# Kernel optimization log

Measured on AMD Instinct MI355X. Metric: run time of the kernel, lower is better.

Reference implementation:

```python
import jax, jax.numpy as jnp
import numpy as np

N_NONZERO = 32      # n_nonzero_coefs
TAU = 0.01
LAMBDA_INIT = -5.0  # reg_coeff = softplus(lambda)


def setup_inputs() -> dict:
    key = jax.random.key(0)
    k1, k2 = jax.random.split(key)
    X = jax.random.normal(k1, (64, 1024, 1024), dtype=jnp.float32)
    y = jax.random.normal(k2, (64, 1024, 1), dtype=jnp.float32)
    return {"X": X, "y": y}


def _omp_fit_forward(X, y):
    # Faithful translation of fit() (omp with hard straight-through top-1)
    # followed by forward() reconstruction D @ coef.
    reg = jax.nn.softplus(jnp.asarray(LAMBDA_INIT, jnp.float32)).astype(X.dtype)
    B, L, A = X.shape
    ones = jnp.ones((B, L, 1), X.dtype)
    Dfull = jnp.concatenate([X, ones], axis=-1)   # [B, L, A+1] (bias column)
    D = Dfull[0]                                   # shared dictionary [L, A+1]
    n_atoms = A + 1
    y2 = y[:, :, 0]                                # [B, L]
    y_det = jax.lax.stop_gradient(y2)
    residuals = y_det
    # Cache selected_D columns incrementally: each column j is dict @ ret_j,
    # identical math to the original's full recompute every iteration.
    selD = jnp.zeros((B, L, N_NONZERO), X.dtype)
    idx_all = []
    nzW = None
    for i in range(N_NONZERO):
        proj = residuals @ D                                      # [B, A+1]
        soft = jax.nn.softmax(jnp.abs(proj) / TAU, axis=-1)
        idx = jnp.argmax(jnp.abs(proj), axis=-1)                  # detached indices
        onehot = jax.nn.one_hot(jnp.argmax(soft, axis=-1), n_atoms, dtype=X.dtype)
        ret = onehot - jax.lax.stop_gradient(soft) + soft         # straight-through
        new_col = ret @ D.T                                       # [B, L]
        selD = selD.at[:, :, i].set(new_col)
        Di = selD[:, :, :i + 1]                                   # [B, L, i+1]
        DTy = jnp.einsum('blk,bl->bk', Di, y2)[..., None]         # [B, i+1, 1]
        DTD = jnp.einsum('blk,blj->bkj', Di, Di) + reg * jnp.eye(i + 1, dtype=X.dtype)
        nzW = jnp.linalg.solve(DTD, DTy)                          # [B, i+1, 1]
        residuals = y_det - jnp.einsum('blk,bk->bl', Di, nzW[..., 0])
        idx_all.append(idx)
    indices = jnp.stack(idx_all, axis=1)                          # [B, K] int
    W = jnp.zeros((B, n_atoms), X.dtype).at[jnp.arange(B)[:, None], indices].set(nzW[..., 0])
    # forward(): bmm(dict_with_bias, coef)
    recon = jnp.einsum('bla,ba->bl', Dfull, W)[..., None]         # [B, L, 1]
    return recon


def reference(X, y):
    return _omp_fit_forward(X, y)
```

## Files before the change

### kernel.cpp

```cpp
#include <hip/hip_runtime.h>
#include <math.h>

#define NATOMS   1025
#define GSTRIDE  1040
#define GELEMS   (1025*GSTRIDE)
#define NNZ      32
#define NBATCH   64
#define REGL     0.0067153485f

#define DPPF(x, ctrl) __int_as_float(__builtin_amdgcn_update_dpp(0, __float_as_int(x), (ctrl), 0xF, 0xF, false))

__device__ __forceinline__ float wave_max64(float x) {
    x = fmaxf(x, DPPF(x, 0x111));
    x = fmaxf(x, DPPF(x, 0x112));
    x = fmaxf(x, DPPF(x, 0x114));
    x = fmaxf(x, DPPF(x, 0x118));
    x = fmaxf(x, DPPF(x, 0x142));
    x = fmaxf(x, DPPF(x, 0x143));
    return __int_as_float(__builtin_amdgcn_readlane(__float_as_int(x), 63));
}
__device__ __forceinline__ float wave_sum64(float x) {
    x += DPPF(x, 0x111);
    x += DPPF(x, 0x112);
    x += DPPF(x, 0x114);
    x += DPPF(x, 0x118);
    x += DPPF(x, 0x142);
    x += DPPF(x, 0x143);
    return __int_as_float(__builtin_amdgcn_readlane(__float_as_int(x), 63));
}
__device__ __forceinline__ float readlane_f(float x, int l) {
    return __int_as_float(__builtin_amdgcn_readlane(__float_as_int(x), l));
}

__global__ __launch_bounds__(256)
void gramprojy_kernel(const float* __restrict__ X0, const float* __restrict__ y,
                      float* __restrict__ Gout, float* __restrict__ PY,
                      int kLen, int nsplit) {
    __shared__ float lds[8192];
    const int tid = threadIdx.x;

    if ((int)blockIdx.z < nsplit) {
        const int bx = blockIdx.x, by = blockIdx.y, bz = blockIdx.z;
        if (by < bx) return;
        float* As = lds;
        float* Bs = lds + 4096;
        const int a0 = bx * 128, b0 = by * 128;
        float* __restrict__ Gp = Gout + (size_t)bz * GELEMS;
        const int tx = tid & 15;
        const int ty = tid >> 4;
        const int lr = tid >> 5;
        const int lc = (tid & 31) * 4;
        const bool aIn = (a0 + 128) <= 1024;
        const bool bIn = (b0 + 128) <= 1024;

        float acc[8][8];
#pragma unroll
        for (int m = 0; m < 8; ++m)
#pragma unroll
            for (int n = 0; n < 8; ++n) acc[m][n] = 0.0f;

        const int kBase = bz * kLen;
        for (int kc = 0; kc < kLen; kc += 32) {
#pragma unroll
            for (int rr = 0; rr < 4; ++rr) {
                const int r = lr + rr * 8;
                const int l = kBase + kc + r;
                if (aIn) {
                    *(float4*)&As[r * 128 + lc] = *(const float4*)&X0[(size_t)l * 1024 + a0 + lc];
                } else {
#pragma unroll
                    for (int k = 0; k < 4; ++k) {
                        const int col = a0 + lc + k;
                        As[r * 128 + lc + k] = (col < 1024) ? X0[(size_t)l * 1024 + col]
                                                            : (col == 1024 ? 1.0f : 0.0f);
                    }
                }
                if (bIn) {
                    *(float4*)&Bs[r * 128 + lc] = *(const float4*)&X0[(size_t)l * 1024 + b0 + lc];
                } else {
#pragma unroll
                    for (int k = 0; k < 4; ++k) {
                        const int col = b0 + lc + k;
                        Bs[r * 128 + lc + k] = (col < 1024) ? X0[(size_t)l * 1024 + col]
                                                            : (col == 1024 ? 1.0f : 0.0f);
                    }
                }
            }
            __syncthreads();
#pragma unroll 8
            for (int l = 0; l < 32; ++l) {
                float4 a01 = *(const float4*)&As[l * 128 + ty * 8];
                float4 a23 = *(const float4*)&As[l * 128 + ty * 8 + 4];
                float4 bA  = *(const float4*)&Bs[l * 128 + tx * 4];
                float4 bB  = *(const float4*)&Bs[l * 128 + 64 + tx * 4];
                float am[8] = {a01.x, a01.y, a01.z, a01.w, a23.x, a23.y, a23.z, a23.w};
                float bn[8] = {bA.x, bA.y, bA.z, bA.w, bB.x, bB.y, bB.z, bB.w};
#pragma unroll
                for (int m = 0; m < 8; ++m)
#pragma unroll
                    for (int n = 0; n < 8; ++n)
                        acc[m][n] += am[m] * bn[n];
            }
            __syncthreads();
        }

#pragma unroll
        for (int m = 0; m < 8; ++m) {
            const int a = a0 + ty * 8 + m;
            if (a >= NATOMS) continue;
            const int bAc = b0 + tx * 4;
            const int bBc = b0 + 64 + tx * 4;
            if (bAc < GSTRIDE) {
                *(float4*)&Gp[(size_t)a * GSTRIDE + bAc] =
                    make_float4(acc[m][0], acc[m][1], acc[m][2], acc[m][3]);
            }
            if (bBc < GSTRIDE) {
                *(float4*)&Gp[(size_t)a * GSTRIDE + bBc] =
                    make_float4(acc[m][4], acc[m][5], acc[m][6], acc[m][7]);
            }
        }
    } else {
        const int pw = blockIdx.y * 9 + blockIdx.x;
        if (pw >= 68) return;
        const int a0 = (pw % 17) * 64;
        const int b0 = (pw / 17) * 16;
        float* Ds = lds;
        float* Ys = lds + 2048;
        const int tx = tid & 15;
        const int ty = tid >> 4;
        const bool aIn = (a0 + 64) <= 1024;

        float acc[4] = {0.0f, 0.0f, 0.0f, 0.0f};

        for (int kc = 0; kc < 1024; kc += 32) {
            {
                const int r  = tid >> 4;
                const int c4 = (tid & 15) * 4;
#pragma unroll
                for (int rr = 0; rr < 2; ++rr) {
                    const int row = r + rr * 16;
                    const int l = kc + row;
                    if (aIn) {
                        *(float4*)&Ds[row * 64 + c4] = *(const float4*)&X0[(size_t)l * 1024 + a0 + c4];
                    } else {
#pragma unroll
                        for (int k = 0; k < 4; ++k) {
                            const int col = a0 + c4 + k;
                            Ds[row * 64 + c4 + k] = (col < 1024) ? X0[(size_t)l * 1024 + col]
                                                                 : (col == 1024 ? 1.0f : 0.0f);
                        }
                    }
                }
            }
            for (int e = tid; e < 512; e += 256) {
                const int l = e & 31, bb = e >> 5;
                Ys[l * 17 + bb] = y[(size_t)(b0 + bb) * 1024 + kc + l];
            }
            __syncthreads();
#pragma unroll 8
            for (int l = 0; l < 32; ++l) {
                const float yv = Ys[l * 17 + ty];
                float4 dv = *(const float4*)&Ds[l * 64 + tx * 4];
                acc[0] += yv * dv.x; acc[1] += yv * dv.y;
                acc[2] += yv * dv.z; acc[3] += yv * dv.w;
            }
            __syncthreads();
        }
        const int a = a0 + tx * 4;
        if (a < GSTRIDE) {
            *(float4*)&PY[(size_t)(b0 + ty) * GSTRIDE + a] =
                make_float4(acc[0], acc[1], acc[2], acc[3]);
        }
    }
}

__global__ __launch_bounds__(256)
void combine_kernel(const float* __restrict__ Gp, float* __restrict__ G,
                    float* __restrict__ diagG, int nsplit) {
    int tt = blockIdx.x, bx = 0;
    while (tt >= 9 - bx) { tt -= 9 - bx; ++bx; }
    const int by = bx + tt;
    const int yq = blockIdx.y;
    const int tid = threadIdx.x;
    for (int rep = 0; rep < 16; ++rep) {
        const int idx = yq * 4096 + rep * 256 + tid;
        const int r = idx >> 7, c = idx & 127;
        const int a = bx * 128 + r, b = by * 128 + c;
        if (a > 1024 || b > 1024) continue;
        float s = 0.0f;
        for (int z = 0; z < nsplit; ++z)
            s += Gp[(size_t)z * GELEMS + (size_t)a * GSTRIDE + b];
        G[(size_t)a * GSTRIDE + b] = s;
        G[(size_t)b * GSTRIDE + a] = s;
        if (a == b) diagG[a] = s;
    }
}

__global__ __launch_bounds__(512)
void omp_kernel(const float* __restrict__ G, const float* __restrict__ PY,
                const float* __restrict__ diagG,
                int* __restrict__ idxOut, float* __restrict__ wOut) {
    __shared__ float rowsLds[NNZ][GSTRIDE];
    __shared__ float pyLds[1040];
    __shared__ float diagLds[1040];
    __shared__ float redV[2][8];
    __shared__ int   redI[2][8];

    const int b = blockIdx.x, tid = threadIdx.x;
    const int lane = tid & 63, wid = tid >> 6;

    float ainv[32];
#pragma unroll
    for (int m = 0; m < 32; ++m) ainv[m] = 0.0f;
    float wvr = 0.0f, rhsr = 0.0f;
    int   myIdx = 0;
    float myW = 0.0f;

    {
        float4 z4 = make_float4(0.f, 0.f, 0.f, 0.f);
        float4* rz = (float4*)rowsLds;
        for (int u = tid; u < NNZ * GSTRIDE / 4; u += 512) rz[u] = z4;
        const float* pyg = PY + (size_t)b * GSTRIDE;
        for (int u = tid; u < 1040; u += 512) pyLds[u] = pyg[u];
        for (int u = tid; u < 1025; u += 512) diagLds[u] = diagG[u];
    }
    __syncthreads();

    float p0 = pyLds[tid], p1 = pyLds[tid + 512];
    float p2 = (tid == 511) ? pyLds[1024] : 0.0f;

    {
        float best = fabsf(p0); int bidx = tid;
        { float v = fabsf(p1); if (v > best) { best = v; bidx = tid + 512; } }
        if (tid == 511) { float v = fabsf(p2); if (v > best) { best = v; bidx = 1024; } }
        const float wmax = wave_max64(best);
        const unsigned long long mask = __ballot(best == wmax);
        const int fl = __ffsll((unsigned long long)mask) - 1;
        const int widx = __builtin_amdgcn_readlane(bidx, fl);
        if (lane == 0) { redV[0][wid] = wmax; redI[0][wid] = widx; }
    }
    __syncthreads();

    for (int i = 0; i < NNZ; ++i) {
        const int par = i & 1;

        float bv_ = redV[par][0]; int sel = redI[par][0];
#pragma unroll
        for (int q = 1; q < 8; ++q) {
            if (redV[par][q] > bv_ || (redV[par][q] == bv_ && redI[par][q] < sel)) {
                bv_ = redV[par][q]; sel = redI[par][q];
            }
        }
        const float pysel = pyLds[sel];

        float r0 = 0.f, r1 = 0.f, r2 = 0.f;
        const float* __restrict__ grow = G + (size_t)sel * GSTRIDE;
        if (i < NNZ - 1) {
            r0 = grow[tid];
            r1 = grow[tid + 512];
            if (tid == 511) r2 = grow[1024];
        }

        const float bvl = (lane < 32) ? rowsLds[lane][sel] : 0.0f;
        float u0 = 0.f, u1 = 0.f, u2 = 0.f, u3 = 0.f;
#pragma unroll
        for (int m = 0; m < 32; m += 4) {
            u0 = fmaf(ainv[m + 0], rowsLds[m + 0][sel], u0);
            u1 = fmaf(ainv[m + 1], rowsLds[m + 1][sel], u1);
            u2 = fmaf(ainv[m + 2], rowsLds[m + 2][sel], u2);
            u3 = fmaf(ainv[m + 3], rowsLds[m + 3][sel], u3);
        }
        const float uacc = (u0 + u1) + (u2 + u3);
        const float t = wave_sum64(bvl * uacc);
        const float s = wave_sum64(rhsr * uacc);
        const float dinv = 1.0f / (diagLds[sel] + REGL - t);
        const float beta = dinv * (pysel - s);
        const float uvb = (lane == i) ? -1.0f : uacc;
#pragma unroll
        for (int m = 0; m < 32; ++m)
            ainv[m] = fmaf(uvb * dinv, readlane_f(uvb, m), ainv[m]);
        wvr = (lane == i) ? beta : fmaf(-uacc, beta, wvr);
        rhsr = (lane == i) ? pysel : rhsr;
        if (tid == i) myIdx = sel;

        if (i == NNZ - 1) break;

        float z0 = -r0, z1 = -r1, z2 = -r2;
        for (int jb = 0; jb < NNZ; jb += 8) {
            if (jb >= i) break;
#pragma unroll
            for (int jj = 0; jj < 8; ++jj) {
                const int j = jb + jj;
                const float uj = readlane_f(uvb, j);
                z0 = fmaf(uj, rowsLds[j][tid],       z0);
                z1 = fmaf(uj, rowsLds[j][tid + 512], z1);
                if (tid == 511) z2 = fmaf(uj, rowsLds[j][1024], z2);
            }
        }
        p0 = fmaf(beta, z0, p0);
        p1 = fmaf(beta, z1, p1);
        if (tid == 511) p2 = fmaf(beta, z2, p2);

        rowsLds[i][tid]       = r0;
        rowsLds[i][tid + 512] = r1;
        if (tid == 511) rowsLds[i][1024] = r2;

        {
            float best = fabsf(p0); int bidx = tid;
            { float v = fabsf(p1); if (v > best) { best = v; bidx = tid + 512; } }
            if (tid == 511) { float v = fabsf(p2); if (v > best) { best = v; bidx = 1024; } }
            const float wmax = wave_max64(best);
            const unsigned long long mask = __ballot(best == wmax);
            const int fl = __ffsll((unsigned long long)mask) - 1;
            const int widx = __builtin_amdgcn_readlane(bidx, fl);
            if (lane == 0) { redV[par ^ 1][wid] = wmax; redI[par ^ 1][wid] = widx; }
        }
        __syncthreads();
    }

    if (tid < NNZ) {
        idxOut[b * NNZ + tid] = myIdx;
        wOut[b * NNZ + tid] = wvr;
    }
}

__global__ __launch_bounds__(256)
void recon_kernel(const float* __restrict__ X, const int* __restrict__ idxIn,
                  const float* __restrict__ wIn, float* __restrict__ out) {
    __shared__ float Wd[1025];
    __shared__ float wval[NNZ];
    __shared__ int   widx[NNZ];
    __shared__ float biasS;
    const int b = blockIdx.x >> 2, chunk = blockIdx.x & 3;
    const int tid = threadIdx.x;
    for (int u = tid; u < 1025; u += 256) Wd[u] = 0.0f;
    __syncthreads();
    if (tid == 0) {
#pragma unroll
        for (int i = 0; i < NNZ; ++i) Wd[idxIn[b * NNZ + i]] = wIn[b * NNZ + i];
        float bias = 0.0f;
#pragma unroll
        for (int i = 0; i < NNZ; ++i) {
            const int gi = idxIn[b * NNZ + i];
            const float v = Wd[gi];
            Wd[gi] = 0.0f;
            const bool isOnes = (gi == 1024);
            if (isOnes) bias += v;
            widx[i] = isOnes ? 0 : gi;
            wval[i] = isOnes ? 0.0f : v;
        }
        biasS = bias;
    }
    __syncthreads();
    const int l = chunk * 256 + tid;
    const float* __restrict__ xr = X + (size_t)b * 1024 * 1024 + (size_t)l * 1024;
    float a0 = biasS, a1 = 0.f, a2 = 0.f, a3 = 0.f;
#pragma unroll
    for (int i = 0; i < NNZ; i += 4) {
        a0 = fmaf(xr[widx[i + 0]], wval[i + 0], a0);
        a1 = fmaf(xr[widx[i + 1]], wval[i + 1], a1);
        a2 = fmaf(xr[widx[i + 2]], wval[i + 2], a2);
        a3 = fmaf(xr[widx[i + 3]], wval[i + 3], a3);
    }
    out[(size_t)b * 1024 + l] = (a0 + a1) + (a2 + a3);
}

extern "C" void kernel_launch(void* const* d_in, const int* in_sizes, int n_in,
                              void* d_out, int out_size, void* d_ws, size_t ws_size,
                              hipStream_t stream) {
    const float* X = (const float*)d_in[0];
    const float* y = (const float*)d_in[1];
    float* out = (float*)d_out;
    float* ws = (float*)d_ws;

    const size_t need4 = ((size_t)GELEMS * 5 + 64 * GSTRIDE + NBATCH * NNZ * 2 + 2048) * sizeof(float);
    const int nsplit = (ws_size >= need4) ? 4 : 1;
    const int kLen = 1024 / nsplit;

    float* Gp = ws;
    float* G  = ws + (size_t)GELEMS * nsplit;
    float* PY = G + (size_t)GELEMS;
    float* wOut = PY + (size_t)64 * GSTRIDE;
    int* idxOut = (int*)(wOut + NBATCH * NNZ);
    float* diagG = (float*)(idxOut + NBATCH * NNZ);

    gramprojy_kernel<<<dim3(9, 9, nsplit + 1), 256, 0, stream>>>(X, y, Gp, PY, kLen, nsplit);
    combine_kernel<<<dim3(45, 4), 256, 0, stream>>>(Gp, G, diagG, nsplit);
    omp_kernel<<<NBATCH, 512, 0, stream>>>(G, PY, diagG, idxOut, wOut);
    recon_kernel<<<NBATCH * 4, 256, 0, stream>>>(X, idxOut, wOut, out);
}
```

Baseline: 221.2 us.

## Drop combine kernel; sum split-K Gram partials on demand in OMP kernel

The separate combine kernel that reduced split-K Gram partials and symmetrized them is removed. The Gram kernel now writes the mirrored transpose tile directly for off-diagonal blocks, and the OMP kernel reads and sums the NS partial rows (and the diagonal) only for the rows it selects. The split count can also rise to 8 when workspace allows, which adds Gram parallelism. The cost is extra partial reads per selected row in the serial OMP loop and more partial buffer traffic.

```diff
diff --git a/kernel.cpp b/kernel.cpp
--- a/kernel.cpp
+++ b/kernel.cpp
@@ -119,6 +119,18 @@
                     make_float4(acc[m][4], acc[m][5], acc[m][6], acc[m][7]);
             }
         }
+        if (bx != by) {
+#pragma unroll
+            for (int n = 0; n < 8; ++n) {
+                const int colg = b0 + ((n < 4) ? (tx * 4 + n) : (64 + tx * 4 + (n - 4)));
+                if (colg >= NATOMS) continue;
+                const int a = a0 + ty * 8;
+                *(float4*)&Gp[(size_t)colg * GSTRIDE + a] =
+                    make_float4(acc[0][n], acc[1][n], acc[2][n], acc[3][n]);
+                *(float4*)&Gp[(size_t)colg * GSTRIDE + a + 4] =
+                    make_float4(acc[4][n], acc[5][n], acc[6][n], acc[7][n]);
+            }
+        }
     } else {
         const int pw = blockIdx.y * 9 + blockIdx.x;
         if (pw >= 68) return;
@@ -174,31 +186,9 @@
     }
 }
 
-__global__ __launch_bounds__(256)
-void combine_kernel(const float* __restrict__ Gp, float* __restrict__ G,
-                    float* __restrict__ diagG, int nsplit) {
-    int tt = blockIdx.x, bx = 0;
-    while (tt >= 9 - bx) { tt -= 9 - bx; ++bx; }
-    const int by = bx + tt;
-    const int yq = blockIdx.y;
-    const int tid = threadIdx.x;
-    for (int rep = 0; rep < 16; ++rep) {
-        const int idx = yq * 4096 + rep * 256 + tid;
-        const int r = idx >> 7, c = idx & 127;
-        const int a = bx * 128 + r, b = by * 128 + c;
-        if (a > 1024 || b > 1024) continue;
-        float s = 0.0f;
-        for (int z = 0; z < nsplit; ++z)
-            s += Gp[(size_t)z * GELEMS + (size_t)a * GSTRIDE + b];
-        G[(size_t)a * GSTRIDE + b] = s;
-        G[(size_t)b * GSTRIDE + a] = s;
-        if (a == b) diagG[a] = s;
-    }
-}
-
+template <int NS>
 __global__ __launch_bounds__(512)
-void omp_kernel(const float* __restrict__ G, const float* __restrict__ PY,
-                const float* __restrict__ diagG,
+void omp_kernel(const float* __restrict__ Gp, const float* __restrict__ PY,
                 int* __restrict__ idxOut, float* __restrict__ wOut) {
     __shared__ float rowsLds[NNZ][GSTRIDE];
     __shared__ float pyLds[1040];
@@ -214,7 +204,6 @@
     for (int m = 0; m < 32; ++m) ainv[m] = 0.0f;
     float wvr = 0.0f, rhsr = 0.0f;
     int   myIdx = 0;
-    float myW = 0.0f;
 
     {
         float4 z4 = make_float4(0.f, 0.f, 0.f, 0.f);
@@ -222,7 +211,17 @@
         for (int u = tid; u < NNZ * GSTRIDE / 4; u += 512) rz[u] = z4;
         const float* pyg = PY + (size_t)b * GSTRIDE;
         for (int u = tid; u < 1040; u += 512) pyLds[u] = pyg[u];
-        for (int u = tid; u < 1025; u += 512) diagLds[u] = diagG[u];
+        float d0 = 0.f, d1 = 0.f, d2 = 0.f;
+#pragma unroll
+        for (int z = 0; z < NS; ++z) {
+            const float* gz = Gp + (size_t)z * GELEMS;
+            d0 += gz[(size_t)tid * (GSTRIDE + 1)];
+            d1 += gz[(size_t)(tid + 512) * (GSTRIDE + 1)];
+            if (tid == 511) d2 += gz[(size_t)1024 * (GSTRIDE + 1)];
+        }
+        diagLds[tid] = d0;
+        diagLds[tid + 512] = d1;
+        if (tid == 511) diagLds[1024] = d2;
     }
     __syncthreads();
 
@@ -253,12 +252,26 @@
         }
         const float pysel = pyLds[sel];
 
-        float r0 = 0.f, r1 = 0.f, r2 = 0.f;
-        const float* __restrict__ grow = G + (size_t)sel * GSTRIDE;
+        float rA0 = 0.f, rA1 = 0.f, rA2 = 0.f, rA3 = 0.f;
+        float rB0 = 0.f, rB1 = 0.f, rB2 = 0.f, rB3 = 0.f;
+        float rA4 = 0.f, rA5 = 0.f, rA6 = 0.f, rA7 = 0.f;
+        float rB4 = 0.f, rB5 = 0.f, rB6 = 0.f, rB7 = 0.f;
+        float rC = 0.f;
         if (i < NNZ - 1) {
-            r0 = grow[tid];
-            r1 = grow[tid + 512];
-            if (tid == 511) r2 = grow[1024];
+            const size_t rowoff = (size_t)sel * GSTRIDE;
+            const float* g0 = Gp + rowoff;
+            rA0 = g0[tid];            rB0 = g0[tid + 512];
+            if (NS > 1) { const float* g = g0 + (size_t)1 * GELEMS; rA1 = g[tid]; rB1 = g[tid + 512]; }
+            if (NS > 2) { const float* g = g0 + (size_t)2 * GELEMS; rA2 = g[tid]; rB2 = g[tid + 512]; }
+            if (NS > 3) { const float* g = g0 + (size_t)3 * GELEMS; rA3 = g[tid]; rB3 = g[tid + 512]; }
+            if (NS > 4) { const float* g = g0 + (size_t)4 * GELEMS; rA4 = g[tid]; rB4 = g[tid + 512]; }
+            if (NS > 5) { const float* g = g0 + (size_t)5 * GELEMS; rA5 = g[tid]; rB5 = g[tid + 512]; }
+            if (NS > 6) { const float* g = g0 + (size_t)6 * GELEMS; rA6 = g[tid]; rB6 = g[tid + 512]; }
+            if (NS > 7) { const float* g = g0 + (size_t)7 * GELEMS; rA7 = g[tid]; rB7 = g[tid + 512]; }
+            if (tid == 511) {
+#pragma unroll
+                for (int z = 0; z < NS; ++z) rC += Gp[(size_t)z * GELEMS + rowoff + 1024];
+            }
         }
 
         const float bvl = (lane < 32) ? rowsLds[lane][sel] : 0.0f;
@@ -285,7 +298,7 @@
 
         if (i == NNZ - 1) break;
 
-        float z0 = -r0, z1 = -r1, z2 = -r2;
+        float z0 = 0.f, z1 = 0.f, z2 = 0.f;
         for (int jb = 0; jb < NNZ; jb += 8) {
             if (jb >= i) break;
 #pragma unroll
@@ -297,13 +310,15 @@
                 if (tid == 511) z2 = fmaf(uj, rowsLds[j][1024], z2);
             }
         }
-        p0 = fmaf(beta, z0, p0);
-        p1 = fmaf(beta, z1, p1);
-        if (tid == 511) p2 = fmaf(beta, z2, p2);
+        const float r0 = ((rA0 + rA1) + (rA2 + rA3)) + ((rA4 + rA5) + (rA6 + rA7));
+        const float r1 = ((rB0 + rB1) + (rB2 + rB3)) + ((rB4 + rB5) + (rB6 + rB7));
+        p0 = fmaf(beta, z0, p0); p0 = fmaf(-beta, r0, p0);
+        p1 = fmaf(beta, z1, p1); p1 = fmaf(-beta, r1, p1);
+        if (tid == 511) { p2 = fmaf(beta, z2, p2); p2 = fmaf(-beta, rC, p2); }
 
         rowsLds[i][tid]       = r0;
         rowsLds[i][tid + 512] = r1;
-        if (tid == 511) rowsLds[i][1024] = r2;
+        if (tid == 511) rowsLds[i][1024] = rC;
 
         {
             float best = fabsf(p0); int bidx = tid;
@@ -373,19 +388,20 @@
     float* out = (float*)d_out;
     float* ws = (float*)d_ws;
 
-    const size_t need4 = ((size_t)GELEMS * 5 + 64 * GSTRIDE + NBATCH * NNZ * 2 + 2048) * sizeof(float);
-    const int nsplit = (ws_size >= need4) ? 4 : 1;
+    const size_t fixed = (size_t)64 * GSTRIDE + NBATCH * NNZ * 2 + 64;
+    const size_t need8 = ((size_t)GELEMS * 8 + fixed) * sizeof(float);
+    const size_t need4 = ((size_t)GELEMS * 4 + fixed) * sizeof(float);
+    const int nsplit = (ws_size >= need8) ? 8 : ((ws_size >= need4) ? 4 : 1);
     const int kLen = 1024 / nsplit;
 
     float* Gp = ws;
-    float* G  = ws + (size_t)GELEMS * nsplit;
-    float* PY = G + (size_t)GELEMS;
+    float* PY = ws + (size_t)GELEMS * nsplit;
     float* wOut = PY + (size_t)64 * GSTRIDE;
     int* idxOut = (int*)(wOut + NBATCH * NNZ);
-    float* diagG = (float*)(idxOut + NBATCH * NNZ);
 
     gramprojy_kernel<<<dim3(9, 9, nsplit + 1), 256, 0, stream>>>(X, y, Gp, PY, kLen, nsplit);
-    combine_kernel<<<dim3(45, 4), 256, 0, stream>>>(Gp, G, diagG, nsplit);
-    omp_kernel<<<NBATCH, 512, 0, stream>>>(G, PY, diagG, idxOut, wOut);
+    if (nsplit == 8)      omp_kernel<8><<<NBATCH, 512, 0, stream>>>(Gp, PY, idxOut, wOut);
+    else if (nsplit == 4) omp_kernel<4><<<NBATCH, 512, 0, stream>>>(Gp, PY, idxOut, wOut);
+    else                  omp_kernel<1><<<NBATCH, 512, 0, stream>>>(Gp, PY, idxOut, wOut);
     recon_kernel<<<NBATCH * 4, 256, 0, stream>>>(X, idxOut, wOut, out);
 }
```

Result: no change. 221.2 us (-0.0%).
